# Kernel tuning notes

Measured on AMD Instinct MI355X. Metric: run time of the kernel, lower is better.

The kernel has to match this reference:

```python
import jax, jax.numpy as jnp
import numpy as np

B, S, E = 2, 4096, 512

def setup_inputs() -> dict:
    key = jax.random.key(0)
    kx, kq, kk, kv, ko = jax.random.split(key, 5)
    scale = 1.0 / np.sqrt(E)  # init-style scaling for weights
    return {
        "x": jax.random.normal(kx, (B, S, E), dtype=jnp.float32),
        "Wq": jax.random.normal(kq, (E, E), dtype=jnp.float32) * scale,
        "Wk": jax.random.normal(kk, (E, E), dtype=jnp.float32) * scale,
        "Wv": jax.random.normal(kv, (E, E), dtype=jnp.float32) * scale,
        "Wo": jax.random.normal(ko, (E, E), dtype=jnp.float32) * scale,
        "bo": jnp.zeros((E,), dtype=jnp.float32),
    }

def reference(x, Wq, Wk, Wv, Wo, bo):
    # nn.Linear: y = x @ W.T  (weights stored [out, in])
    q = jnp.einsum("bse,fe->bsf", x, Wq)
    k = jnp.einsum("bse,fe->bsf", x, Wk)
    v = jnp.einsum("bse,fe->bsf", x, Wv)
    inv_scale = 1.0 / jnp.sqrt(jnp.asarray(x.shape[-1], x.dtype))
    scores = jnp.einsum("bqe,bke->bqk", q, k) * inv_scale  # [B,S,S]
    S_len = x.shape[1]
    # torch.triu(ones) keeps j >= i; masked_fill where triu==0 masks j < i
    row = jnp.arange(S_len)[:, None]
    col = jnp.arange(S_len)[None, :]
    keep = col >= row  # [S,S], faithfully anti-causal as in the source
    scores = jnp.where(keep[None, :, :], scores, jnp.asarray(-jnp.inf, scores.dtype))
    attn = jax.nn.softmax(scores, axis=-1)
    # dropout p=0.0 -> identity
    out = jnp.einsum("bqk,bke->bqe", attn, v)
    return jnp.einsum("bse,fe->bsf", out, Wo) + bo
```

## Files before the change

kernel.cpp:

```cpp
#include <hip/hip_runtime.h>
#include <hip/hip_bf16.h>

#define S_LEN 4096
#define E_DIM 512
#define B_DIM 2
#define M_ROWS (B_DIM * S_LEN)

typedef __attribute__((ext_vector_type(8))) short short8;
typedef __attribute__((ext_vector_type(4))) float floatx4;

__device__ __forceinline__ unsigned short f2bf(float f) {
    unsigned u = __float_as_uint(f);
    unsigned r = (u + 0x7fffu + ((u >> 16) & 1u)) >> 16;
    return (unsigned short)r;
}
__device__ __forceinline__ float bf2f(unsigned short u) {
    return __uint_as_float((unsigned)u << 16);
}

__device__ __forceinline__ void async_copy16(unsigned short* lds, const unsigned short* g) {
    auto gp = (const __attribute__((address_space(1))) unsigned int*)g;
    auto lp = (__attribute__((address_space(3))) unsigned int*)lds;
    __builtin_amdgcn_global_load_lds(gp, lp, 16, 0, 0);
}

struct MapArg { unsigned short m[576]; };

__global__ __launch_bounds__(256) void convert_bf16(
    const float* __restrict__ x,  const float* __restrict__ wq,
    const float* __restrict__ wk, const float* __restrict__ wv,
    const float* __restrict__ wo, unsigned short* __restrict__ dstU,
    unsigned short* __restrict__ dstWo)
{
    long i = (long)blockIdx.x * 1024 + (long)threadIdx.x * 4;
    const float* src; long off; unsigned short* dst; long doff;
    if      (i < 4194304) { src = x;  off = i;           dst = dstU;  doff = i; }
    else if (i < 4456448) { src = wq; off = i - 4194304; dst = dstU;  doff = i; }
    else if (i < 4718592) { src = wk; off = i - 4456448; dst = dstU;  doff = i; }
    else if (i < 4980736) { src = wv; off = i - 4718592; dst = dstU;  doff = i; }
    else                  { src = wo; off = i - 4980736; dst = dstWo; doff = i - 4980736; }
    float4 v = *(const float4*)(src + off);
    ushort4 o;
    o.x = f2bf(v.x); o.y = f2bf(v.y); o.z = f2bf(v.z); o.w = f2bf(v.w);
    *(ushort4*)(dst + doff) = o;
}

__device__ __forceinline__ void gemm_core(
    const unsigned short* __restrict__ A, const unsigned short* __restrict__ W,
    void* __restrict__ Cv, const float* __restrict__ bias, int mode,
    int m0, int n0)
{
    __shared__ unsigned short As[128 * 32];
    __shared__ unsigned short Bs[128 * 32];
    const int tid = threadIdx.x;
    const int lane = tid & 63, wave = tid >> 6;
    const int wm = wave >> 1, wn = wave & 1;
    const int q4 = lane >> 4, l16 = lane & 15;

    floatx4 acc[4][4];
#pragma unroll
    for (int i = 0; i < 4; ++i)
#pragma unroll
        for (int j = 0; j < 4; ++j) acc[i][j] = (floatx4){0.f, 0.f, 0.f, 0.f};

    const int srow = lane >> 2;
    const int scol = (lane & 3) * 8;

    for (int k0 = 0; k0 < 512; k0 += 32) {
        async_copy16(&As[(wave * 16) * 32],
                     A + (size_t)(m0 + wave * 16 + srow) * 512 + k0 + scol);
        async_copy16(&As[(64 + wave * 16) * 32],
                     A + (size_t)(m0 + 64 + wave * 16 + srow) * 512 + k0 + scol);
        async_copy16(&Bs[(wave * 16) * 32],
                     W + (size_t)(n0 + wave * 16 + srow) * 512 + k0 + scol);
        async_copy16(&Bs[(64 + wave * 16) * 32],
                     W + (size_t)(n0 + 64 + wave * 16 + srow) * 512 + k0 + scol);
        __syncthreads();
        short8 af[4], bfr[4];
#pragma unroll
        for (int i = 0; i < 4; ++i) {
            af[i]  = *(const short8*)&As[(wm * 64 + i * 16 + l16) * 32 + q4 * 8];
            bfr[i] = *(const short8*)&Bs[(wn * 64 + i * 16 + l16) * 32 + q4 * 8];
        }
#pragma unroll
        for (int i = 0; i < 4; ++i)
#pragma unroll
            for (int j = 0; j < 4; ++j)
                acc[i][j] = __builtin_amdgcn_mfma_f32_16x16x32_bf16(af[i], bfr[j], acc[i][j], 0, 0, 0);
        __syncthreads();
    }

    if (mode == 0) {
        unsigned short* C = (unsigned short*)Cv;
#pragma unroll
        for (int i = 0; i < 4; ++i) {
            int rowb = m0 + wm * 64 + i * 16 + q4 * 4;
#pragma unroll
            for (int j = 0; j < 4; ++j) {
                int col = n0 + wn * 64 + j * 16 + l16;
#pragma unroll
                for (int rg = 0; rg < 4; ++rg)
                    C[(size_t)(rowb + rg) * 512 + col] = f2bf(acc[i][j][rg]);
            }
        }
    } else if (mode == 1) {
        unsigned short* C = (unsigned short*)Cv;
#pragma unroll
        for (int i = 0; i < 4; ++i) {
            int grow = m0 + wm * 64 + i * 16 + q4 * 4;
            int b = grow >> 12, s = grow & 4095;
#pragma unroll
            for (int j = 0; j < 4; ++j) {
                int e = n0 + wn * 64 + j * 16 + l16;
                ushort4 pk;
                pk.x = f2bf(acc[i][j][0]); pk.y = f2bf(acc[i][j][1]);
                pk.z = f2bf(acc[i][j][2]); pk.w = f2bf(acc[i][j][3]);
                *(ushort4*)(C + (size_t)b * 512 * 4096 + (size_t)e * 4096 + s) = pk;
            }
        }
    } else {
        float* C = (float*)Cv;
#pragma unroll
        for (int i = 0; i < 4; ++i) {
            int rowb = m0 + wm * 64 + i * 16 + q4 * 4;
#pragma unroll
            for (int j = 0; j < 4; ++j) {
                int col = n0 + wn * 64 + j * 16 + l16;
                float bv = bias[col];
#pragma unroll
                for (int rg = 0; rg < 4; ++rg)
                    C[(size_t)(rowb + rg) * 512 + col] = acc[i][j][rg] + bv;
            }
        }
    }
}

__global__ __launch_bounds__(256) void gemm_qkv(
    const unsigned short* __restrict__ xb,
    const unsigned short* __restrict__ Wqb, const unsigned short* __restrict__ Wkb,
    const unsigned short* __restrict__ Wvb,
    unsigned short* __restrict__ Qb, unsigned short* __restrict__ Kb,
    unsigned short* __restrict__ Vtb)
{
    const int z = blockIdx.z;
    const unsigned short* W = (z == 0) ? Wqb : (z == 1) ? Wkb : Wvb;
    unsigned short* C = (z == 0) ? Qb : (z == 1) ? Kb : Vtb;
    gemm_core(xb, W, C, nullptr, (z == 2) ? 1 : 0, blockIdx.y * 128, blockIdx.x * 128);
}

__global__ __launch_bounds__(256) void gemm_out(
    const unsigned short* __restrict__ AOb, const unsigned short* __restrict__ Wob,
    const float* __restrict__ bo, float* __restrict__ out)
{
    gemm_core(AOb, Wob, out, bo, 2, blockIdx.y * 128, blockIdx.x * 128);
}

__global__ __launch_bounds__(512, 2) void flash_mfma(
    const unsigned short* __restrict__ Qg, const unsigned short* __restrict__ Kg,
    const unsigned short* __restrict__ Vt,
    unsigned short* __restrict__ Oh, float* __restrict__ Lb, MapArg map)
{
    const int enc = map.m[blockIdx.x];
    const int tile = enc & 63, ch = (enc >> 6) & 7, bb = enc >> 9;
    const int i0 = tile * 64;
    const int lo0 = 512 * ch, hi = lo0 + 512;
    const int lo = (i0 > lo0) ? i0 : lo0;
    const int lo_al = lo & ~127;
    const int nsteps = (hi - lo_al) >> 7;

    const int tid = threadIdx.x;
    const int lane = tid & 63, w = tid >> 6;
    const int q4 = lane >> 4, l16 = lane & 15;
    const int e = l16 & 7;
    const float scale = 0.044194173824159216f;
    const float MREF = 4.0f;

    __shared__ unsigned short Qs[64 * 512];
    __shared__ unsigned short Plds[2][64][136];
    __shared__ float Lred[8][64];

    const size_t rowbase = (size_t)bb * S_LEN;
    const size_t vbase   = (size_t)bb * (size_t)512 * 4096;

#pragma unroll
    for (int rr = 0; rr < 8; ++rr) {
        const int row = w * 8 + rr;
        const unsigned short* src = Qg + (rowbase + i0 + row) * 512
                                    + ((lane ^ (row & 7)) << 3);
        async_copy16(&Qs[row * 512], src);
    }

    floatx4 oacc[4][4];
#pragma unroll
    for (int mg = 0; mg < 4; ++mg)
#pragma unroll
        for (int nc = 0; nc < 4; ++nc) oacc[mg][nc] = (floatx4){0.f, 0.f, 0.f, 0.f};
    float l_acc[4] = {0.f, 0.f, 0.f, 0.f};

    const unsigned short* qb0 = &Qs[l16 * 512 + ((q4 ^ e) << 3)];
    const unsigned short* qb1 = &Qs[l16 * 512 + (((q4 + 4) ^ e) << 3)];
    const unsigned short* kpbase = Kg + (rowbase + 16 * w + l16) * 512 + (q4 << 3);

    __syncthreads();

    for (int t = 0; t < nsteps; ++t) {
        const int j0 = lo_al + t * 128;
        const int buf = t & 1;

        short8 kf[16];
        const unsigned short* kp = kpbase + (size_t)j0 * 512;
#pragma unroll
        for (int ks = 0; ks < 16; ++ks)
            kf[ks] = *(const short8*)(kp + ks * 32);

        floatx4 sf[4];
#pragma unroll
        for (int mg = 0; mg < 4; ++mg) sf[mg] = (floatx4){0.f, 0.f, 0.f, 0.f};
        __builtin_amdgcn_s_setprio(1);
#pragma unroll
        for (int ks = 0; ks < 16; ++ks) {
            const unsigned short* qb = (ks & 1) ? qb1 : qb0;
#pragma unroll
            for (int mg = 0; mg < 4; ++mg) {
                short8 a = *(const short8*)(qb + mg * 8192 + (ks >> 1) * 64);
                sf[mg] = __builtin_amdgcn_mfma_f32_16x16x32_bf16(kf[ks], a, sf[mg], 0, 0, 0);
            }
        }
        __builtin_amdgcn_s_setprio(0);

        short8 vf[4][4];
#pragma unroll
        for (int nc = 0; nc < 4; ++nc) {
            const unsigned short* vpn = Vt + vbase
                + (size_t)(w * 64 + nc * 16 + l16) * 4096 + j0 + (q4 << 3);
#pragma unroll
            for (int kslot = 0; kslot < 4; ++kslot)
                vf[nc][kslot] = *(const short8*)(vpn + kslot * 32);
        }

        const int kb = j0 + 16 * w + (q4 << 2);
        const bool full = (j0 >= i0 + 64);
#pragma unroll
        for (int mg = 0; mg < 4; ++mg) {
            const int row = i0 + mg * 16 + l16;
            float p0 = __expf(sf[mg][0] * scale - MREF);
            float p1 = __expf(sf[mg][1] * scale - MREF);
            float p2 = __expf(sf[mg][2] * scale - MREF);
            float p3 = __expf(sf[mg][3] * scale - MREF);
            if (!full) {
                p0 = (kb + 0 >= row) ? p0 : 0.f;
                p1 = (kb + 1 >= row) ? p1 : 0.f;
                p2 = (kb + 2 >= row) ? p2 : 0.f;
                p3 = (kb + 3 >= row) ? p3 : 0.f;
            }
            l_acc[mg] += p0 + p1 + p2 + p3;
            ushort4 pk;
            pk.x = f2bf(p0); pk.y = f2bf(p1); pk.z = f2bf(p2); pk.w = f2bf(p3);
            *(ushort4*)&Plds[buf][mg * 16 + l16][16 * w + (q4 << 2)] = pk;
        }
        __syncthreads();

        __builtin_amdgcn_s_setprio(1);
#pragma unroll
        for (int kslot = 0; kslot < 4; ++kslot) {
#pragma unroll
            for (int mg = 0; mg < 4; ++mg) {
                short8 ap = *(const short8*)&Plds[buf][mg * 16 + l16][kslot * 32 + (q4 << 3)];
#pragma unroll
                for (int nc = 0; nc < 4; ++nc)
                    oacc[mg][nc] = __builtin_amdgcn_mfma_f32_16x16x32_bf16(
                        ap, vf[nc][kslot], oacc[mg][nc], 0, 0, 0);
            }
        }
        __builtin_amdgcn_s_setprio(0);
    }

#pragma unroll
    for (int mg = 0; mg < 4; ++mg) {
        float v = l_acc[mg];
        v += __shfl_xor(v, 16, 64);
        v += __shfl_xor(v, 32, 64);
        if (q4 == 0) Lred[w][mg * 16 + l16] = v;
    }
    __syncthreads();

    const int slot = 8 * ch * (ch + 1) + bb * 8 * (ch + 1) + tile;
    if (tid < 64) {
        float sum = 0.f;
#pragma unroll
        for (int ww = 0; ww < 8; ++ww) sum += Lred[ww][tid];
        Lb[(size_t)slot * 64 + tid] = sum;
    }

    unsigned short* Op = Oh + (size_t)slot * 64 * 512;
#pragma unroll
    for (int mg = 0; mg < 4; ++mg)
#pragma unroll
        for (int nc = 0; nc < 4; ++nc)
#pragma unroll
            for (int rg = 0; rg < 4; ++rg)
                Op[(size_t)(mg * 16 + q4 * 4 + rg) * 512 + w * 64 + nc * 16 + l16]
                    = f2bf(oacc[mg][nc][rg]);
}

__global__ __launch_bounds__(256) void flash_merge(
    const unsigned short* __restrict__ Oh, const float* __restrict__ Lb,
    unsigned short* __restrict__ AO)
{
    const int row = blockIdx.x;
    const int c = threadIdx.x * 2;
    const int bb = row >> 12, i = row & 4095;
    const int t = i >> 6, ri = i & 63;
    const int chmin = i >> 9;
    float lsum = 0.f, v0 = 0.f, v1 = 0.f;
    for (int ch = chmin; ch < 8; ++ch) {
        int slot = 8 * ch * (ch + 1) + bb * 8 * (ch + 1) + t;
        lsum += Lb[(size_t)slot * 64 + ri];
        const unsigned short* p = Oh + (size_t)slot * 64 * 512 + (size_t)ri * 512 + c;
        v0 += bf2f(p[0]);
        v1 += bf2f(p[1]);
    }
    float inv = 1.f / lsum;
    ushort2 o; o.x = f2bf(v0 * inv); o.y = f2bf(v1 * inv);
    *(ushort2*)(AO + (size_t)row * 512 + c) = o;
}

static MapArg build_map() {
    int enc[576], steps[576], n = 0;
    for (int bb = 0; bb < 2; ++bb)
        for (int ch = 0; ch < 8; ++ch)
            for (int t = 0; t < 8 * (ch + 1); ++t) {
                int i0 = t * 64, lo0 = 512 * ch, hi = lo0 + 512;
                int lo = (i0 > lo0) ? i0 : lo0;
                int lo_al = lo & ~127;
                enc[n] = t | (ch << 6) | (bb << 9);
                steps[n] = (hi - lo_al) >> 7;
                ++n;
            }
    MapArg mp{};
    int idx = 0;
    for (int sv = 4; sv >= 1; --sv)
        for (int i = 0; i < n; ++i)
            if (steps[i] == sv) mp.m[idx++] = (unsigned short)enc[i];
    return mp;
}

extern "C" void kernel_launch(void* const* d_in, const int* in_sizes, int n_in,
                              void* d_out, int out_size, void* d_ws, size_t ws_size,
                              hipStream_t stream) {
    (void)in_sizes; (void)n_in; (void)out_size; (void)ws_size;
    const float* x  = (const float*)d_in[0];
    const float* Wq = (const float*)d_in[1];
    const float* Wk = (const float*)d_in[2];
    const float* Wv = (const float*)d_in[3];
    const float* Wo = (const float*)d_in[4];
    const float* bo = (const float*)d_in[5];
    float* out = (float*)d_out;

    unsigned short* ws  = (unsigned short*)d_ws;
    unsigned short* Wob = ws;
    unsigned short* QAb = ws + 262144;
    unsigned short* Kb  = QAb + 4194304;
    unsigned short* Vtb = Kb + 4194304;
    unsigned short* U   = Vtb + 4194304;
    unsigned short* xb  = U;
    unsigned short* Wqb = U + 4194304;
    unsigned short* Wkb = Wqb + 262144;
    unsigned short* Wvb = Wkb + 262144;
    unsigned short* Ohb = U;
    float* Lbf = (float*)(U + 18874368);

    static const MapArg mp = build_map();

    convert_bf16<<<5120, 256, 0, stream>>>(x, Wq, Wk, Wv, Wo, U, Wob);

    gemm_qkv<<<dim3(4, 64, 3), 256, 0, stream>>>(xb, Wqb, Wkb, Wvb, QAb, Kb, Vtb);

    flash_mfma<<<576, 512, 0, stream>>>(QAb, Kb, Vtb, Ohb, Lbf, mp);

    flash_merge<<<8192, 256, 0, stream>>>(Ohb, Lbf, QAb);

    gemm_out<<<dim3(4, 64), 256, 0, stream>>>(QAb, Wob, bo, out);
}
```

Measured before the change: 215.5 us.

## Prefetch next K/V register tiles and remap blocks per XCD for balance

The attention loop now loads the next step's K fragments during the softmax phase and the next V fragments after the PV MFMAs, so global load latency overlaps compute instead of stalling at the start of each step. The __syncthreads is replaced by an explicit lgkmcnt wait plus s_barrier, so the in-flight global prefetches are not drained at the barrier. The block map is rebuilt so each of 8 interleaved slots pairs a long and a short chunk per batch, sorted by step count, spreading work evenly across XCDs. This costs more live registers for the kf/vf double use and may lower occupancy.

Measured after the change: 234.4 us. +8.8%, slower.

```diff
diff --git a/kernel.cpp b/kernel.cpp
--- a/kernel.cpp
+++ b/kernel.cpp
@@ -200,18 +200,30 @@
     const unsigned short* qb0 = &Qs[l16 * 512 + ((q4 ^ e) << 3)];
     const unsigned short* qb1 = &Qs[l16 * 512 + (((q4 + 4) ^ e) << 3)];
     const unsigned short* kpbase = Kg + (rowbase + 16 * w + l16) * 512 + (q4 << 3);
+    const unsigned short* vpbase = Vt + vbase + (size_t)(w * 64 + l16) * 4096 + (q4 << 3);
+
+    short8 kf[16];
+    {
+        const unsigned short* kp = kpbase + (size_t)lo_al * 512;
+#pragma unroll
+        for (int ks = 0; ks < 16; ++ks)
+            kf[ks] = *(const short8*)(kp + ks * 32);
+    }
+    short8 vf[4][4];
+#pragma unroll
+    for (int nc = 0; nc < 4; ++nc) {
+        const unsigned short* vpn = vpbase + (size_t)(nc * 16) * 4096 + lo_al;
+#pragma unroll
+        for (int kslot = 0; kslot < 4; ++kslot)
+            vf[nc][kslot] = *(const short8*)(vpn + kslot * 32);
+    }
 
     __syncthreads();
 
     for (int t = 0; t < nsteps; ++t) {
         const int j0 = lo_al + t * 128;
+        const int jp = (t + 1 < nsteps) ? j0 + 128 : j0;
         const int buf = t & 1;
-
-        short8 kf[16];
-        const unsigned short* kp = kpbase + (size_t)j0 * 512;
-#pragma unroll
-        for (int ks = 0; ks < 16; ++ks)
-            kf[ks] = *(const short8*)(kp + ks * 32);
 
         floatx4 sf[4];
 #pragma unroll
@@ -228,14 +240,11 @@
         }
         __builtin_amdgcn_s_setprio(0);
 
-        short8 vf[4][4];
-#pragma unroll
-        for (int nc = 0; nc < 4; ++nc) {
-            const unsigned short* vpn = Vt + vbase
-                + (size_t)(w * 64 + nc * 16 + l16) * 4096 + j0 + (q4 << 3);
-#pragma unroll
-            for (int kslot = 0; kslot < 4; ++kslot)
-                vf[nc][kslot] = *(const short8*)(vpn + kslot * 32);
+        {
+            const unsigned short* kp = kpbase + (size_t)jp * 512;
+#pragma unroll
+            for (int ks = 0; ks < 16; ++ks)
+                kf[ks] = *(const short8*)(kp + ks * 32);
         }
 
         const int kb = j0 + 16 * w + (q4 << 2);
@@ -258,7 +267,10 @@
             pk.x = f2bf(p0); pk.y = f2bf(p1); pk.z = f2bf(p2); pk.w = f2bf(p3);
             *(ushort4*)&Plds[buf][mg * 16 + l16][16 * w + (q4 << 2)] = pk;
         }
-        __syncthreads();
+
+        asm volatile("s_waitcnt lgkmcnt(0)" ::: "memory");
+        __builtin_amdgcn_s_barrier();
+        __builtin_amdgcn_sched_barrier(0);
 
         __builtin_amdgcn_s_setprio(1);
 #pragma unroll
@@ -273,6 +285,14 @@
             }
         }
         __builtin_amdgcn_s_setprio(0);
+
+#pragma unroll
+        for (int nc = 0; nc < 4; ++nc) {
+            const unsigned short* vpn = vpbase + (size_t)(nc * 16) * 4096 + jp;
+#pragma unroll
+            for (int kslot = 0; kslot < 4; ++kslot)
+                vf[nc][kslot] = *(const short8*)(vpn + kslot * 32);
+        }
     }
 
 #pragma unroll
@@ -326,22 +346,29 @@
 }
 
 static MapArg build_map() {
-    int enc[576], steps[576], n = 0;
-    for (int bb = 0; bb < 2; ++bb)
-        for (int ch = 0; ch < 8; ++ch)
+    MapArg mp{};
+    for (int x = 0; x < 8; ++x) {
+        const int bb = x >> 2;
+        const int chs[2] = {7 - (x & 3), x & 3};
+        int enc[72], st[72], n = 0;
+        for (int ci = 0; ci < 2; ++ci) {
+            const int ch = chs[ci];
             for (int t = 0; t < 8 * (ch + 1); ++t) {
                 int i0 = t * 64, lo0 = 512 * ch, hi = lo0 + 512;
                 int lo = (i0 > lo0) ? i0 : lo0;
                 int lo_al = lo & ~127;
                 enc[n] = t | (ch << 6) | (bb << 9);
-                steps[n] = (hi - lo_al) >> 7;
+                st[n] = (hi - lo_al) >> 7;
                 ++n;
             }
-    MapArg mp{};
-    int idx = 0;
-    for (int sv = 4; sv >= 1; --sv)
-        for (int i = 0; i < n; ++i)
-            if (steps[i] == sv) mp.m[idx++] = (unsigned short)enc[i];
+        }
+        for (int i = 1; i < n; ++i) {
+            int ev = enc[i], sv = st[i], j = i - 1;
+            while (j >= 0 && st[j] < sv) { st[j + 1] = st[j]; enc[j + 1] = enc[j]; --j; }
+            st[j + 1] = sv; enc[j + 1] = ev;
+        }
+        for (int j = 0; j < n; ++j) mp.m[x + 8 * j] = (unsigned short)enc[j];
+    }
     return mp;
 }
 
```
